# Kernel optimization log

Measured on AMD Instinct MI355X. Metric: run time of the kernel, lower is better.

The kernel has to match this reference:

```python
import jax, jax.numpy as jnp
import numpy as np

B, NQ, NK = 1, 2048, 2048
A_DIM = M_DIM = 1024
H, KD, VD = 16, 64, 64


def setup_inputs() -> dict:
    key = jax.random.key(0)
    ks = jax.random.split(key, 8)
    return {
        "q_data": jax.random.normal(ks[0], (B, NQ, A_DIM), jnp.float32),
        "m_data": jax.random.normal(ks[1], (B, NK, M_DIM), jnp.float32),
        "batched_bias": jax.random.normal(ks[2], (B, H, NQ, NK), jnp.float32),
        "query_w": jax.random.normal(ks[3], (A_DIM, H, KD), jnp.float32) * 0.02,
        "query_b": jax.random.normal(ks[4], (1, H, KD), jnp.float32) * 0.02,
        "key_w": jax.random.normal(ks[5], (M_DIM, H, KD), jnp.float32) * 0.02,
        "value_w": jax.random.normal(ks[6], (M_DIM, H, VD), jnp.float32) * 0.02,
        "gating_w": jax.random.normal(ks[7], (A_DIM, H, VD), jnp.float32) * 0.02,
    }


def reference(q_data, m_data, batched_bias, query_w, query_b, key_w, value_w, gating_w):
    key_dim = query_w.shape[-1]
    scale = key_dim ** -0.5
    # fused: QKV projections + query bias + pair bias + softmax + gating
    q = (jnp.einsum('bqa,ahc->bqhc', q_data, query_w) + query_b) * scale  # [B,Q,H,KD]
    k = jnp.einsum('bka,ahc->bkhc', m_data, key_w)                        # [B,K,H,KD]
    v = jnp.einsum('bka,ahc->bkhc', m_data, value_w)                      # [B,K,H,VD]
    logits = jnp.einsum('bqhc,bkhc->bhqk', q, k) + batched_bias           # [B,H,Q,K]
    weights = jax.nn.softmax(logits, axis=-1)
    weighted = jnp.einsum('bhqk,bkhc->bqhc', weights, v)                  # [B,Q,H,VD]
    gate = jax.nn.sigmoid(jnp.einsum('bqa,ahc->bqhc', q_data, gating_w))  # [B,Q,H,VD]
    return gate * weighted
```

## Files before the change

### kernel.cpp

```cpp
#include <hip/hip_runtime.h>
#include <hip/hip_bf16.h>

typedef __bf16 bf16x8 __attribute__((ext_vector_type(8)));
typedef __bf16 bf16x4 __attribute__((ext_vector_type(4)));
typedef float  f32x4  __attribute__((ext_vector_type(4)));

typedef const __attribute__((address_space(1))) void* gptr_t;
typedef __attribute__((address_space(3))) void*       lptr_t;

#define NQ 2048
#define NK 2048
#define AD 1024
#define NH 16
#define HD 64
#define HC 1024

__global__ __launch_bounds__(256) void prep_convert(
    const float* __restrict__ q_data, const float* __restrict__ m_data,
    __bf16* __restrict__ aq, __bf16* __restrict__ am) {
  const int NEL4 = NQ * AD / 4;
  int gid = blockIdx.x * 256 + threadIdx.x;
  float4 v;
  __bf16* dst;
  if (gid < NEL4) { v = ((const float4*)q_data)[gid]; dst = aq + (size_t)gid * 4; }
  else            { v = ((const float4*)m_data)[gid - NEL4]; dst = am + (size_t)(gid - NEL4) * 4; }
  bf16x4 o;
  o[0] = (__bf16)v.x; o[1] = (__bf16)v.y; o[2] = (__bf16)v.z; o[3] = (__bf16)v.w;
  *(bf16x4*)dst = o;
}

__global__ __launch_bounds__(256) void prep_transpose(
    const float* __restrict__ w0, const float* __restrict__ w1,
    const float* __restrict__ w2, const float* __restrict__ w3,
    __bf16* __restrict__ t0, __bf16* __restrict__ t1,
    __bf16* __restrict__ t2, __bf16* __restrict__ t3) {
  __shared__ float tile[64][65];
  int b = blockIdx.x;
  int wsel = b >> 8;
  int t = b & 255;
  int a0 = (t >> 4) * 64, n0 = (t & 15) * 64;
  const float* W = (wsel == 0) ? w0 : (wsel == 1) ? w1 : (wsel == 2) ? w2 : w3;
  __bf16*      T = (wsel == 0) ? t0 : (wsel == 1) ? t1 : (wsel == 2) ? t2 : t3;
  int tx = threadIdx.x & 63, ty = threadIdx.x >> 6;
#pragma unroll
  for (int r = 0; r < 64; r += 4)
    tile[ty + r][tx] = W[(size_t)(a0 + ty + r) * HC + n0 + tx];
  __syncthreads();
#pragma unroll
  for (int r = 0; r < 64; r += 4)
    T[(size_t)(n0 + ty + r) * AD + a0 + tx] = (__bf16)tile[tx][ty + r];
}

__global__ __launch_bounds__(256) void proj_gemm(
    const __bf16* __restrict__ Aq, const __bf16* __restrict__ Am,
    const __bf16* __restrict__ Wq, const __bf16* __restrict__ Wk,
    const __bf16* __restrict__ Wv, const __bf16* __restrict__ Wg,
    const float* __restrict__ qbias,
    __bf16* __restrict__ qbf, __bf16* __restrict__ kb,
    __bf16* __restrict__ vt, float* __restrict__ gate) {
  __shared__ __bf16 As[128 * 32];
  __shared__ __bf16 Bs[128 * 32];
  int bx = blockIdx.x;
  int mode = bx >> 7, t = bx & 127;
  const __bf16 *A, *B;
  int bm, bn;
  if (mode == 2) {
    A = Wv; B = Am; bm = (t >> 4) << 7; bn = (t & 15) << 7;
  } else {
    bm = (t >> 3) << 7; bn = (t & 7) << 7;
    A = (mode == 1) ? Am : Aq;
    B = (mode == 0) ? Wq : (mode == 1) ? Wk : Wg;
  }
  int lane = threadIdx.x & 63, wave = threadIdx.x >> 6;
  int quad = lane >> 4, l15 = lane & 15;
  int wm = (wave >> 1) << 6, wn = (wave & 1) << 6;
  int srow = lane >> 2, schunk = lane & 3;

  f32x4 acc[4][4] = {};

  for (int k0 = 0; k0 < AD; k0 += 32) {
#pragma unroll
    for (int i = 0; i < 2; i++) {
      int inst = wave * 2 + i;
      int row = inst * 16 + srow;
      __builtin_amdgcn_global_load_lds(
          (gptr_t)((const char*)A + ((size_t)(bm + row) * AD + k0) * 2 + schunk * 16),
          (lptr_t)(As + inst * 512), 16, 0, 0);
      __builtin_amdgcn_global_load_lds(
          (gptr_t)((const char*)B + ((size_t)(bn + row) * AD + k0) * 2 + schunk * 16),
          (lptr_t)(Bs + inst * 512), 16, 0, 0);
    }
    __syncthreads();
    bf16x8 af[4], bfr[4];
#pragma unroll
    for (int i = 0; i < 4; i++) af[i]  = *(const bf16x8*)(As + (wm + i * 16 + l15) * 32 + quad * 8);
#pragma unroll
    for (int j = 0; j < 4; j++) bfr[j] = *(const bf16x8*)(Bs + (wn + j * 16 + l15) * 32 + quad * 8);
#pragma unroll
    for (int i = 0; i < 4; i++)
#pragma unroll
      for (int j = 0; j < 4; j++)
        acc[i][j] = __builtin_amdgcn_mfma_f32_16x16x32_bf16(af[i], bfr[j], acc[i][j], 0, 0, 0);
    __syncthreads();
  }

#pragma unroll
  for (int j = 0; j < 4; j++) {
    int n = bn + wn + j * 16 + l15;
    float qbb = (mode == 0) ? qbias[n] : 0.f;
#pragma unroll
    for (int i = 0; i < 4; i++) {
#pragma unroll
      for (int r = 0; r < 4; r++) {
        int m = bm + wm + i * 16 + quad * 4 + r;
        float v = acc[i][j][r];
        if (mode == 0) {
          int h = n >> 6, c = n & 63;
          qbf[((size_t)h * NQ + m) * HD + c] = (__bf16)((v + qbb) * 0.125f);
        } else if (mode == 1) {
          int h = n >> 6, c = n & 63;
          kb[((size_t)h * NK + m) * HD + c] = (__bf16)v;
        } else if (mode == 2) {
          vt[(size_t)m * NK + n] = (__bf16)v;
        } else {
          gate[(size_t)m * HC + n] = 1.f / (1.f + __expf(-v));
        }
      }
    }
  }
}

__global__ __launch_bounds__(256, 2) void attn(
    const __bf16* __restrict__ qbuf, const __bf16* __restrict__ kbuf,
    const __bf16* __restrict__ vtb, const float* __restrict__ gate,
    const float* __restrict__ bias, float* __restrict__ out) {
  __shared__ __bf16 Kt[2][128 * 64];
  __shared__ __bf16 Vt[2][64 * 128];
  __shared__ __bf16 P_lds[4][16 * 68];

  int bx = blockIdx.x;
  int h = bx & 15, qb0 = bx >> 4;
  int lane = threadIdx.x & 63, wave = threadIdx.x >> 6;
  int quad = lane >> 4, l15 = lane & 15;
  int qrow = (qb0 << 6) + wave * 16;

  const __bf16* qh = qbuf + (size_t)h * NQ * HD;
  const __bf16* kh = kbuf + (size_t)h * NK * HD;
  const __bf16* vh = vtb + (size_t)h * HD * NK;
  const float*  bh = bias + (size_t)h * NQ * NK;

  bf16x8 a_q[2];
#pragma unroll
  for (int kk = 0; kk < 2; kk++)
    a_q[kk] = *(const bf16x8*)(qh + (size_t)(qrow + l15) * HD + quad * 8 + kk * 32);

  float lpart[4] = {0.f, 0.f, 0.f, 0.f};
  f32x4 acc_o[4] = {};
  __bf16* pl = &P_lds[wave][0];

  int srowK = lane >> 3;
  int srowV = lane >> 4;
#define STAGE(bufi, k0s)                                                      \
  {                                                                           \
    _Pragma("unroll")                                                         \
    for (int j = 0; j < 4; j++) {                                             \
      int i = wave * 4 + j;                                                   \
      int rK = i * 8 + srowK;                                                 \
      int cK = (lane & 7) ^ ((2 * i + (srowK >> 2)) & 7);                     \
      __builtin_amdgcn_global_load_lds(                                       \
          (gptr_t)(kh + (size_t)(k0s + rK) * 64 + cK * 8),                    \
          (lptr_t)(&Kt[bufi][i * 512]), 16, 0, 0);                            \
      int rV = i * 4 + srowV;                                                 \
      int cV = (lane & 15) ^ ((i * 4 + srowV) & 15);                          \
      __builtin_amdgcn_global_load_lds(                                       \
          (gptr_t)(vh + (size_t)rV * NK + k0s + cV * 8),                      \
          (lptr_t)(&Vt[bufi][i * 512]), 16, 0, 0);                            \
    }                                                                         \
  }

  STAGE(0, 0)

  f32x4 spc[8];
#pragma unroll
  for (int s = 0; s < 2; s++)
#pragma unroll
    for (int r = 0; r < 4; r++)
      spc[s * 4 + r] = *(const f32x4*)(bh + (size_t)(qrow + quad * 4 + r) * NK + s * 64 + 4 * l15);

  for (int t = 0; t < 16; ++t) {
    int buf = t & 1;
    __syncthreads();

    if (t < 15) STAGE(buf ^ 1, (t + 1) * 128)

    f32x4 s2[2][4];
#pragma unroll
    for (int s = 0; s < 2; s++)
#pragma unroll
      for (int jt = 0; jt < 4; jt++)
#pragma unroll
        for (int r = 0; r < 4; r++)
          s2[s][jt][r] = spc[s * 4 + r][jt];

    if (t < 15) {
      const float* bn_ = bh + (size_t)(t + 1) * 128;
#pragma unroll
      for (int s = 0; s < 2; s++)
#pragma unroll
        for (int r = 0; r < 4; r++)
          spc[s * 4 + r] = *(const f32x4*)(bn_ + (size_t)(qrow + quad * 4 + r) * NK + s * 64 + 4 * l15);
    }

    const __bf16* Kb = &Kt[buf][0];
    const __bf16* Vb = &Vt[buf][0];

#pragma unroll
    for (int s = 0; s < 2; s++) {
      bf16x8 b_k[4][2];
#pragma unroll
      for (int jt = 0; jt < 4; jt++)
#pragma unroll
        for (int kk = 0; kk < 2; kk++) {
          int R = s * 64 + 4 * l15 + jt;
          int pc = (quad + 4 * kk) ^ (l15 & 7);
          b_k[jt][kk] = *(const bf16x8*)(Kb + R * 64 + pc * 8);
        }

#pragma unroll
      for (int jt = 0; jt < 4; jt++)
#pragma unroll
        for (int kk = 0; kk < 2; kk++)
          s2[s][jt] = __builtin_amdgcn_mfma_f32_16x16x32_bf16(a_q[kk], b_k[jt][kk], s2[s][jt], 0, 0, 0);

#pragma unroll
      for (int r = 0; r < 4; r++) {
        bf16x4 w;
#pragma unroll
        for (int jt = 0; jt < 4; jt++) {
          float pv = __expf(s2[s][jt][r]);
          lpart[r] += pv;
          w[jt] = (__bf16)pv;
        }
        *(bf16x4*)(pl + (quad * 4 + r) * 68 + 4 * l15) = w;
      }

      bf16x8 a_p[2];
#pragma unroll
      for (int kk = 0; kk < 2; kk++) {
        const __bf16* src = pl + l15 * 68 + quad * 8 + kk * 32;
        bf16x4 lo = *(const bf16x4*)src;
        bf16x4 hi = *(const bf16x4*)(src + 4);
        bf16x8 a;
#pragma unroll
        for (int j = 0; j < 4; j++) { a[j] = lo[j]; a[4 + j] = hi[j]; }
        a_p[kk] = a;
      }

      bf16x8 b_v[4][2];
#pragma unroll
      for (int jt = 0; jt < 4; jt++)
#pragma unroll
        for (int kk = 0; kk < 2; kk++) {
          int R = jt * 16 + l15;
          int pc = (s * 8 + kk * 4 + quad) ^ l15;
          b_v[jt][kk] = *(const bf16x8*)(Vb + R * 128 + pc * 8);
        }

#pragma unroll
      for (int jt = 0; jt < 4; jt++)
#pragma unroll
        for (int kk = 0; kk < 2; kk++)
          acc_o[jt] = __builtin_amdgcn_mfma_f32_16x16x32_bf16(a_p[kk], b_v[jt][kk], acc_o[jt], 0, 0, 0);
    }
  }

#pragma unroll
  for (int off = 1; off < 16; off <<= 1)
#pragma unroll
    for (int r = 0; r < 4; r++) lpart[r] += __shfl_xor(lpart[r], off);
  float inv[4];
#pragma unroll
  for (int r = 0; r < 4; r++) inv[r] = 1.f / lpart[r];
#pragma unroll
  for (int jt = 0; jt < 4; jt++)
#pragma unroll
    for (int r = 0; r < 4; r++) {
      int q = qrow + quad * 4 + r;
      int d = jt * 16 + l15;
      float g = gate[(size_t)q * HC + h * HD + d];
      out[((size_t)q * NH + h) * HD + d] = acc_o[jt][r] * inv[r] * g;
    }
}

extern "C" void kernel_launch(void* const* d_in, const int* in_sizes, int n_in,
                              void* d_out, int out_size, void* d_ws, size_t ws_size,
                              hipStream_t stream) {
  const float* q_data   = (const float*)d_in[0];
  const float* m_data   = (const float*)d_in[1];
  const float* bias     = (const float*)d_in[2];
  const float* query_w  = (const float*)d_in[3];
  const float* query_b  = (const float*)d_in[4];
  const float* key_w    = (const float*)d_in[5];
  const float* value_w  = (const float*)d_in[6];
  const float* gating_w = (const float*)d_in[7];
  float* out = (float*)d_out;

  char* ws = (char*)d_ws;
  __bf16* Aq   = (__bf16*)(ws);
  __bf16* Am   = (__bf16*)(ws + ((size_t)4 << 20));
  __bf16* Wq   = (__bf16*)(ws + ((size_t)8 << 20));
  __bf16* Wk   = (__bf16*)(ws + ((size_t)10 << 20));
  __bf16* Wv   = (__bf16*)(ws + ((size_t)12 << 20));
  __bf16* Wg   = (__bf16*)(ws + ((size_t)14 << 20));
  __bf16* qbuf = (__bf16*)(ws + ((size_t)16 << 20));
  __bf16* kbuf = (__bf16*)(ws + ((size_t)20 << 20));
  __bf16* vtb  = (__bf16*)(ws + ((size_t)24 << 20));
  float*  gbuf = (float*)(ws + ((size_t)28 << 20));

  prep_convert<<<4096, 256, 0, stream>>>(q_data, m_data, Aq, Am);
  prep_transpose<<<1024, 256, 0, stream>>>(query_w, key_w, value_w, gating_w, Wq, Wk, Wv, Wg);
  proj_gemm<<<512, 256, 0, stream>>>(Aq, Am, Wq, Wk, Wv, Wg, query_b, qbuf, kbuf, vtb, gbuf);
  attn<<<512, 256, 0, stream>>>(qbuf, kbuf, vtb, gbuf, bias, out);
}
```

Measured before the change: 437.9 us.

## Fuse prep kernels, double-buffer projection GEMM LDS, raise MFMA wave priority

The two preprocessing kernels are merged into one launch that picks its job from the block index. The projection GEMM gets double-buffered LDS so the next k-tile's global-to-LDS load is issued while the current tile is being multiplied, which drops one barrier per iteration. s_setprio is wrapped around the MFMA blocks in both the GEMM and the attention kernel to favour waves issuing matrix work. The cost is twice the LDS in the GEMM, which may lower occupancy.

New measurement: 434.6 us. No clear change (-0.8%).

```diff
diff --git a/kernel.cpp b/kernel.cpp
--- a/kernel.cpp
+++ b/kernel.cpp
@@ -15,27 +15,27 @@
 #define HD 64
 #define HC 1024
 
-__global__ __launch_bounds__(256) void prep_convert(
+__global__ __launch_bounds__(256) void prep_fused(
     const float* __restrict__ q_data, const float* __restrict__ m_data,
-    __bf16* __restrict__ aq, __bf16* __restrict__ am) {
-  const int NEL4 = NQ * AD / 4;
-  int gid = blockIdx.x * 256 + threadIdx.x;
-  float4 v;
-  __bf16* dst;
-  if (gid < NEL4) { v = ((const float4*)q_data)[gid]; dst = aq + (size_t)gid * 4; }
-  else            { v = ((const float4*)m_data)[gid - NEL4]; dst = am + (size_t)(gid - NEL4) * 4; }
-  bf16x4 o;
-  o[0] = (__bf16)v.x; o[1] = (__bf16)v.y; o[2] = (__bf16)v.z; o[3] = (__bf16)v.w;
-  *(bf16x4*)dst = o;
-}
-
-__global__ __launch_bounds__(256) void prep_transpose(
+    __bf16* __restrict__ aq, __bf16* __restrict__ am,
     const float* __restrict__ w0, const float* __restrict__ w1,
     const float* __restrict__ w2, const float* __restrict__ w3,
     __bf16* __restrict__ t0, __bf16* __restrict__ t1,
     __bf16* __restrict__ t2, __bf16* __restrict__ t3) {
   __shared__ float tile[64][65];
-  int b = blockIdx.x;
+  if (blockIdx.x < 4096) {
+    const int NEL4 = NQ * AD / 4;
+    int gid = blockIdx.x * 256 + threadIdx.x;
+    float4 v;
+    __bf16* dst;
+    if (gid < NEL4) { v = ((const float4*)q_data)[gid]; dst = aq + (size_t)gid * 4; }
+    else            { v = ((const float4*)m_data)[gid - NEL4]; dst = am + (size_t)(gid - NEL4) * 4; }
+    bf16x4 o;
+    o[0] = (__bf16)v.x; o[1] = (__bf16)v.y; o[2] = (__bf16)v.z; o[3] = (__bf16)v.w;
+    *(bf16x4*)dst = o;
+    return;
+  }
+  int b = blockIdx.x - 4096;
   int wsel = b >> 8;
   int t = b & 255;
   int a0 = (t >> 4) * 64, n0 = (t & 15) * 64;
@@ -58,8 +58,8 @@
     const float* __restrict__ qbias,
     __bf16* __restrict__ qbf, __bf16* __restrict__ kb,
     __bf16* __restrict__ vt, float* __restrict__ gate) {
-  __shared__ __bf16 As[128 * 32];
-  __shared__ __bf16 Bs[128 * 32];
+  __shared__ __bf16 As[2][128 * 32];
+  __shared__ __bf16 Bs[2][128 * 32];
   int bx = blockIdx.x;
   int mode = bx >> 7, t = bx & 127;
   const __bf16 *A, *B;
@@ -78,30 +78,40 @@
 
   f32x4 acc[4][4] = {};
 
-  for (int k0 = 0; k0 < AD; k0 += 32) {
-#pragma unroll
-    for (int i = 0; i < 2; i++) {
-      int inst = wave * 2 + i;
-      int row = inst * 16 + srow;
-      __builtin_amdgcn_global_load_lds(
-          (gptr_t)((const char*)A + ((size_t)(bm + row) * AD + k0) * 2 + schunk * 16),
-          (lptr_t)(As + inst * 512), 16, 0, 0);
-      __builtin_amdgcn_global_load_lds(
-          (gptr_t)((const char*)B + ((size_t)(bn + row) * AD + k0) * 2 + schunk * 16),
-          (lptr_t)(Bs + inst * 512), 16, 0, 0);
-    }
+#define PSTAGE(bufi, k0s)                                                     \
+  {                                                                           \
+    _Pragma("unroll")                                                         \
+    for (int i = 0; i < 2; i++) {                                             \
+      int inst = wave * 2 + i;                                                \
+      int row = inst * 16 + srow;                                             \
+      __builtin_amdgcn_global_load_lds(                                       \
+          (gptr_t)((const char*)A + ((size_t)(bm + row) * AD + (k0s)) * 2 + schunk * 16), \
+          (lptr_t)(&As[bufi][inst * 512]), 16, 0, 0);                         \
+      __builtin_amdgcn_global_load_lds(                                       \
+          (gptr_t)((const char*)B + ((size_t)(bn + row) * AD + (k0s)) * 2 + schunk * 16), \
+          (lptr_t)(&Bs[bufi][inst * 512]), 16, 0, 0);                         \
+    }                                                                         \
+  }
+
+  PSTAGE(0, 0)
+
+  for (int kt = 0; kt < 32; ++kt) {
+    int buf = kt & 1;
     __syncthreads();
+    if (kt < 31) PSTAGE(buf ^ 1, (kt + 1) * 32)
+
     bf16x8 af[4], bfr[4];
 #pragma unroll
-    for (int i = 0; i < 4; i++) af[i]  = *(const bf16x8*)(As + (wm + i * 16 + l15) * 32 + quad * 8);
-#pragma unroll
-    for (int j = 0; j < 4; j++) bfr[j] = *(const bf16x8*)(Bs + (wn + j * 16 + l15) * 32 + quad * 8);
+    for (int i = 0; i < 4; i++) af[i]  = *(const bf16x8*)(&As[buf][(wm + i * 16 + l15) * 32 + quad * 8]);
+#pragma unroll
+    for (int j = 0; j < 4; j++) bfr[j] = *(const bf16x8*)(&Bs[buf][(wn + j * 16 + l15) * 32 + quad * 8]);
+    __builtin_amdgcn_s_setprio(1);
 #pragma unroll
     for (int i = 0; i < 4; i++)
 #pragma unroll
       for (int j = 0; j < 4; j++)
         acc[i][j] = __builtin_amdgcn_mfma_f32_16x16x32_bf16(af[i], bfr[j], acc[i][j], 0, 0, 0);
-    __syncthreads();
+    __builtin_amdgcn_s_setprio(0);
   }
 
 #pragma unroll
@@ -226,11 +236,13 @@
           b_k[jt][kk] = *(const bf16x8*)(Kb + R * 64 + pc * 8);
         }
 
+      __builtin_amdgcn_s_setprio(1);
 #pragma unroll
       for (int jt = 0; jt < 4; jt++)
 #pragma unroll
         for (int kk = 0; kk < 2; kk++)
           s2[s][jt] = __builtin_amdgcn_mfma_f32_16x16x32_bf16(a_q[kk], b_k[jt][kk], s2[s][jt], 0, 0, 0);
+      __builtin_amdgcn_s_setprio(0);
 
 #pragma unroll
       for (int r = 0; r < 4; r++) {
@@ -266,11 +278,13 @@
           b_v[jt][kk] = *(const bf16x8*)(Vb + R * 128 + pc * 8);
         }
 
+      __builtin_amdgcn_s_setprio(1);
 #pragma unroll
       for (int jt = 0; jt < 4; jt++)
 #pragma unroll
         for (int kk = 0; kk < 2; kk++)
           acc_o[jt] = __builtin_amdgcn_mfma_f32_16x16x32_bf16(a_p[kk], b_v[jt][kk], acc_o[jt], 0, 0, 0);
+      __builtin_amdgcn_s_setprio(0);
     }
   }
 
@@ -317,8 +331,9 @@
   __bf16* vtb  = (__bf16*)(ws + ((size_t)24 << 20));
   float*  gbuf = (float*)(ws + ((size_t)28 << 20));
 
-  prep_convert<<<4096, 256, 0, stream>>>(q_data, m_data, Aq, Am);
-  prep_transpose<<<1024, 256, 0, stream>>>(query_w, key_w, value_w, gating_w, Wq, Wk, Wv, Wg);
+  prep_fused<<<5120, 256, 0, stream>>>(q_data, m_data, Aq, Am,
+                                       query_w, key_w, value_w, gating_w,
+                                       Wq, Wk, Wv, Wg);
   proj_gemm<<<512, 256, 0, stream>>>(Aq, Am, Wq, Wk, Wv, Wg, query_b, qbuf, kbuf, vtb, gbuf);
   attn<<<512, 256, 0, stream>>>(qbuf, kbuf, vtb, gbuf, bias, out);
 }
```
